# Performance work log

Hardware: AMD Instinct MI355X
Metric: run time of the kernel (lower is better)

The kernel has to match this reference:

```python
import jax, jax.numpy as jnp
import numpy as np

BS, LQ = 16, 300
D, NH = 256, 8
HD = D // NH
NLAYERS, DFF = 6, 1024
NLVL, NPTS = 4, 4
SUMP = NLVL * NPTS  # total sampling points per head
SPATIAL = [(80, 80), (40, 40), (20, 20), (10, 10)]
LEN_V = sum(h * w for h, w in SPATIAL)  # 8500
OFFSET_SCALE = 0.5


def layer_norm(x, g, b, eps=1e-5):
    m = jnp.mean(x, -1, keepdims=True)
    v = jnp.mean((x - m) ** 2, -1, keepdims=True)
    return (x - m) * jax.lax.rsqrt(v + eps) * g + b


def bilinear_gather(v, loc, Hs, Ws):
    # v: [bs, nh, Hs*Ws, hd]; loc: [bs, nh, N, 2] in [0,1] (x, y)
    # grid_sample bilinear, align_corners=False, zero padding
    x = loc[..., 0] * Ws - 0.5
    y = loc[..., 1] * Hs - 0.5
    x0 = jnp.floor(x); y0 = jnp.floor(y)
    x1 = x0 + 1.0; y1 = y0 + 1.0
    wx1 = x - x0; wx0 = 1.0 - wx1
    wy1 = y - y0; wy0 = 1.0 - wy1

    def corner(xi, yi, w):
        valid = (xi >= 0) & (xi <= Ws - 1) & (yi >= 0) & (yi <= Hs - 1)
        idx = (jnp.clip(yi, 0, Hs - 1) * Ws + jnp.clip(xi, 0, Ws - 1)).astype(jnp.int32)
        g = jnp.take_along_axis(v, idx[..., None], axis=2)  # [bs,nh,N,hd]
        return g * (w * valid)[..., None]

    return (corner(x0, y0, wx0 * wy0) + corner(x1, y0, wx1 * wy0)
            + corner(x0, y1, wx0 * wy1) + corner(x1, y1, wx1 * wy1))


def ms_deform_attn(value, loc, attn_w):
    # value [bs,LenV,D]; loc [bs,Lq,nh,SUMP,2]; attn_w [bs,Lq,nh,SUMP]
    bs, Lq = loc.shape[:2]
    v = value.reshape(bs, -1, NH, HD).transpose(0, 2, 1, 3)  # [bs,nh,LenV,hd]
    sizes = [h * w for h, w in SPATIAL]
    offs = np.cumsum([0] + sizes)
    outs = []
    for lvl, (Hs, Ws) in enumerate(SPATIAL):
        v_l = v[:, :, offs[lvl]:offs[lvl + 1], :]
        loc_l = loc[:, :, :, lvl * NPTS:(lvl + 1) * NPTS, :]
        loc_l = loc_l.transpose(0, 2, 1, 3, 4).reshape(bs, NH, Lq * NPTS, 2)
        s = bilinear_gather(v_l, loc_l, Hs, Ws).reshape(bs, NH, Lq, NPTS, HD)
        outs.append(s)
    samp = jnp.concatenate(outs, axis=3)  # [bs,nh,Lq,SUMP,hd]
    w = attn_w.transpose(0, 2, 1, 3)[..., None]
    out = jnp.sum(samp * w, axis=3)  # [bs,nh,Lq,hd]
    return out.transpose(0, 2, 1, 3).reshape(bs, Lq, D)


def mha(q_in, k_in, v_in, Wqkv, bqkv, Wo, bo):
    # torch nn.MultiheadAttention (batch_first), no dropout, no mask
    bs, Lq, _ = q_in.shape
    Wq, Wk, Wv = jnp.split(Wqkv, 3, axis=0)
    bq, bk, bv = jnp.split(bqkv, 3)
    q = (q_in @ Wq.T + bq).reshape(bs, Lq, NH, HD)
    k = (k_in @ Wk.T + bk).reshape(bs, -1, NH, HD)
    v = (v_in @ Wv.T + bv).reshape(bs, -1, NH, HD)
    scores = jnp.einsum('bqhd,bkhd->bhqk', q, k) / jnp.sqrt(jnp.float32(HD))
    a = jax.nn.softmax(scores, axis=-1)
    o = jnp.einsum('bhqk,bkhd->bqhd', a, v).reshape(bs, Lq, D)
    return o @ Wo.T + bo


def _forward(target, reference_points, value, query_pos_embed,
             attn_Wqkv, attn_bqkv, attn_Wo, attn_bo, n1_g, n1_b,
             so_W, so_b, aw_W, aw_b, g_W, g_b, gn_g, gn_b,
             l1_W, l1_b, l2_W, l2_b, n3_g, n3_b):
    bs, Lq = target.shape[:2]
    # num_points_scale = 1/n_points per point (all levels use NPTS points)
    nps = jnp.full((SUMP, 1), 1.0 / NPTS, dtype=target.dtype)
    t = target
    for i in range(NLAYERS):
        # self-attention
        q = t + query_pos_embed
        t2 = mha(q, q, t, attn_Wqkv[i], attn_bqkv[i], attn_Wo[i], attn_bo[i])
        t = layer_norm(t + t2, n1_g[i], n1_b[i])
        # MS deformable cross-attention (4-dim reference_points branch)
        qc = t + query_pos_embed
        so = (qc @ so_W[i].T + so_b[i]).reshape(bs, Lq, NH, SUMP, 2)
        aw = jax.nn.softmax((qc @ aw_W[i].T + aw_b[i]).reshape(bs, Lq, NH, SUMP), axis=-1)
        ref = reference_points[:, :, None, None, :]  # [bs,Lq,1,1,4]
        loc = ref[..., :2] + so * nps * ref[..., 2:] * OFFSET_SCALE
        t2 = ms_deform_attn(value, loc, aw)
        # gateway fusion
        gates = jax.nn.sigmoid(jnp.concatenate([t, t2], -1) @ g_W[i].T + g_b[i])
        g1, g2 = jnp.split(gates, 2, axis=-1)
        t = layer_norm(g1 * t + g2 * t2, gn_g[i], gn_b[i])
        # FFN
        t2 = jax.nn.relu(t @ l1_W[i].T + l1_b[i]) @ l2_W[i].T + l2_b[i]
        t = layer_norm(jnp.clip(t + t2, -65504.0, 65504.0), n3_g[i], n3_b[i])
    return t


def setup_inputs() -> dict:
    key = jax.random.key(0)
    ks = iter(jax.random.split(key, 40))

    def rn(shape, s=0.02):
        return jax.random.normal(next(ks), shape, dtype=jnp.float32) * s

    inp = {
        'target': jax.random.normal(next(ks), (BS, LQ, D), dtype=jnp.float32),
        'reference_points': jax.random.uniform(next(ks), (BS, LQ, 4), dtype=jnp.float32) * 0.5 + 0.25,
        'value': jax.random.normal(next(ks), (BS, LEN_V, D), dtype=jnp.float32),
        'query_pos_embed': jax.random.normal(next(ks), (BS, LQ, D), dtype=jnp.float32),
        'attn_Wqkv': rn((NLAYERS, 3 * D, D)),
        'attn_bqkv': jnp.zeros((NLAYERS, 3 * D), jnp.float32),
        'attn_Wo': rn((NLAYERS, D, D)),
        'attn_bo': jnp.zeros((NLAYERS, D), jnp.float32),
        'n1_g': jnp.ones((NLAYERS, D), jnp.float32),
        'n1_b': jnp.zeros((NLAYERS, D), jnp.float32),
        'so_W': rn((NLAYERS, NH * SUMP * 2, D)),
        'so_b': rn((NLAYERS, NH * SUMP * 2), 0.5),
        'aw_W': rn((NLAYERS, NH * SUMP, D)),
        'aw_b': jnp.zeros((NLAYERS, NH * SUMP), jnp.float32),
        'g_W': rn((NLAYERS, 2 * D, 2 * D)),
        'g_b': jnp.zeros((NLAYERS, 2 * D), jnp.float32),
        'gn_g': jnp.ones((NLAYERS, D), jnp.float32),
        'gn_b': jnp.zeros((NLAYERS, D), jnp.float32),
        'l1_W': rn((NLAYERS, DFF, D)),
        'l1_b': jnp.zeros((NLAYERS, DFF), jnp.float32),
        'l2_W': rn((NLAYERS, D, DFF)),
        'l2_b': jnp.zeros((NLAYERS, D), jnp.float32),
        'n3_g': jnp.ones((NLAYERS, D), jnp.float32),
        'n3_b': jnp.zeros((NLAYERS, D), jnp.float32),
    }
    return inp


def reference(target, reference_points, value, query_pos_embed,
              attn_Wqkv, attn_bqkv, attn_Wo, attn_bo, n1_g, n1_b,
              so_W, so_b, aw_W, aw_b, g_W, g_b, gn_g, gn_b,
              l1_W, l1_b, l2_W, l2_b, n3_g, n3_b):
    return _forward(target, reference_points, value, query_pos_embed,
                    attn_Wqkv, attn_bqkv, attn_Wo, attn_bo, n1_g, n1_b,
                    so_W, so_b, aw_W, aw_b, g_W, g_b, gn_g, gn_b,
                    l1_W, l1_b, l2_W, l2_b, n3_g, n3_b)
```

## Files before the change

kernel.cpp:

```cpp
#include <hip/hip_runtime.h>

#define BS 16
#define LQ 300
#define D 256
#define NH 8
#define HD 32
#define DFF 1024
#define ROWS (BS*LQ)
#define LEN_V 8500

typedef __attribute__((ext_vector_type(8))) short short8;
typedef __attribute__((ext_vector_type(4))) float f32x4;

__device__ __forceinline__ uint32_t bf16r(float x)
{
    const uint32_t u = __float_as_uint(x);
    return (u + 0x7fffu + ((u >> 16) & 1u)) >> 16;
}
__device__ __forceinline__ float lof(uint32_t p) { return __uint_as_float(p << 16); }
__device__ __forceinline__ float hif(uint32_t p) { return __uint_as_float(p & 0xffff0000u); }

template<int ACT>
__global__ __launch_bounds__(256)
void gemm_mfma(const float* __restrict__ A, int lda,
               const float* __restrict__ A2, int lda2, int ksplit,
               const float* __restrict__ W,
               const float* __restrict__ bias,
               float* __restrict__ C, int ldc, int coff,
               int K)
{
    __shared__ __align__(16) unsigned short As[64*64];
    __shared__ __align__(16) unsigned short Bs[64*64];
    const int tid  = threadIdx.x;
    const int bm   = blockIdx.x, bn = blockIdx.y;
    const int lane = tid & 63;
    const int w    = tid >> 6;
    const int wm   = (w >> 1) * 32, wn = (w & 1) * 32;
    const int fr   = lane & 15;
    const int fq   = lane >> 4;

    const int srow = tid >> 2;
    const int sg   = tid & 3;

    f32x4 acc[2][2] = {};

    for (int k0 = 0; k0 < K; k0 += 64) {
        float4 a0[2], a1[2], w0[2], w1[2];
#pragma unroll
        for (int p = 0; p < 2; ++p) {
            const int grp = sg + 4*p;
            const int kg  = k0 + grp*8;
            const float* Asrc = (A2 != nullptr && kg >= ksplit)
                ? (A2 + (size_t)(bm*64 + srow)*lda2 + (kg - ksplit))
                : (A  + (size_t)(bm*64 + srow)*lda  + kg);
            a0[p] = *reinterpret_cast<const float4*>(Asrc);
            a1[p] = *reinterpret_cast<const float4*>(Asrc + 4);
            const float* Wsrc = W + (size_t)(bn*64 + srow)*K + kg;
            w0[p] = *reinterpret_cast<const float4*>(Wsrc);
            w1[p] = *reinterpret_cast<const float4*>(Wsrc + 4);
        }
        __syncthreads();
#pragma unroll
        for (int p = 0; p < 2; ++p) {
            const int grp  = sg + 4*p;
            const int slot = grp ^ (srow & 7);
            uint32_t pk[4];
            pk[0] = bf16r(a0[p].x) | (bf16r(a0[p].y) << 16);
            pk[1] = bf16r(a0[p].z) | (bf16r(a0[p].w) << 16);
            pk[2] = bf16r(a1[p].x) | (bf16r(a1[p].y) << 16);
            pk[3] = bf16r(a1[p].z) | (bf16r(a1[p].w) << 16);
            *reinterpret_cast<uint4*>(&As[srow*64 + slot*8]) =
                make_uint4(pk[0], pk[1], pk[2], pk[3]);
            pk[0] = bf16r(w0[p].x) | (bf16r(w0[p].y) << 16);
            pk[1] = bf16r(w0[p].z) | (bf16r(w0[p].w) << 16);
            pk[2] = bf16r(w1[p].x) | (bf16r(w1[p].y) << 16);
            pk[3] = bf16r(w1[p].z) | (bf16r(w1[p].w) << 16);
            *reinterpret_cast<uint4*>(&Bs[srow*64 + slot*8]) =
                make_uint4(pk[0], pk[1], pk[2], pk[3]);
        }
        __syncthreads();
#pragma unroll
        for (int ks = 0; ks < 2; ++ks) {
            short8 af[2], bf[2];
#pragma unroll
            for (int fm = 0; fm < 2; ++fm) {
                const int row = wm + fm*16 + fr;
                const int slot = (ks*4 + fq) ^ (row & 7);
                af[fm] = *reinterpret_cast<const short8*>(&As[row*64 + slot*8]);
            }
#pragma unroll
            for (int fn = 0; fn < 2; ++fn) {
                const int row = wn + fn*16 + fr;
                const int slot = (ks*4 + fq) ^ (row & 7);
                bf[fn] = *reinterpret_cast<const short8*>(&Bs[row*64 + slot*8]);
            }
#pragma unroll
            for (int fm = 0; fm < 2; ++fm)
#pragma unroll
                for (int fn = 0; fn < 2; ++fn)
                    acc[fm][fn] = __builtin_amdgcn_mfma_f32_16x16x32_bf16(
                        af[fm], bf[fn], acc[fm][fn], 0, 0, 0);
        }
    }

#pragma unroll
    for (int fm = 0; fm < 2; ++fm)
#pragma unroll
        for (int fn = 0; fn < 2; ++fn) {
            const int col = bn*64 + wn + fn*16 + fr;
            const float bia = bias[col];
#pragma unroll
            for (int r = 0; r < 4; ++r) {
                const int row = bm*64 + wm + fm*16 + fq*4 + r;
                float v = acc[fm][fn][r] + bia;
                if (ACT == 1) v = fmaxf(v, 0.f);
                if (ACT == 2) v = 1.f / (1.f + __expf(-v));
                C[(size_t)row*ldc + coff + col] = v;
            }
        }
}

__global__ __launch_bounds__(256)
void add_pos(const float* __restrict__ t, const float* __restrict__ pos,
             float* __restrict__ q)
{
    const size_t idx = (size_t)blockIdx.x*256 + threadIdx.x;
    q[idx] = t[idx] + pos[idx];
}

__global__ __launch_bounds__(256)
void mha_block(const float* __restrict__ qkv, float* __restrict__ o)
{
    const int blk = blockIdx.x;
    const int quarter = blk & 3;
    const int bh = blk >> 2;
    const int b = bh >> 3, h = bh & 7;
    const int tid = threadIdx.x;
    const int lane = tid & 63;
    const int w = tid >> 6;

    __shared__ uint32_t Kp[16][320];
    __shared__ uint32_t Vp[150][32];
    __shared__ float    ws[4][304];
    const float* base = qkv + (size_t)b * LQ * 768;
    const int hc = h * 32;

    for (int idx = tid; idx < 300*16; idx += 256) {
        const int j = idx >> 4, d2 = idx & 15;
        const float2 kv = *reinterpret_cast<const float2*>(base + (size_t)j*768 + 256 + hc + 2*d2);
        Kp[d2][j] = (bf16r(kv.y) << 16) | bf16r(kv.x);
    }
    for (int idx = tid; idx < 16*20; idx += 256)
        Kp[idx/20][300 + idx%20] = 0;
    for (int idx = tid; idx < 150*32; idx += 256) {
        const int jp = idx >> 5, d = idx & 31;
        const float lo = base[(size_t)(2*jp  )*768 + 512 + hc + d];
        const float hi = base[(size_t)(2*jp+1)*768 + 512 + hc + d];
        Vp[jp][d] = (bf16r(hi) << 16) | bf16r(lo);
    }
    __syncthreads();

    const float scale = 0.17677669529663687f;
    const int qbase = quarter * 75;
    for (int il = w; il < 75; il += 4) {
        const int iq = qbase + il;
        const float2* qrow = reinterpret_cast<const float2*>(base + (size_t)iq*768 + hc);

        float s0=0.f, s1=0.f, s2=0.f, s3=0.f, s4=0.f;
#pragma unroll
        for (int d2 = 0; d2 < 16; ++d2) {
            const float2 q2 = qrow[d2];
            uint32_t k;
            k = Kp[d2][lane      ]; s0 += lof(k)*q2.x + hif(k)*q2.y;
            k = Kp[d2][lane +  64]; s1 += lof(k)*q2.x + hif(k)*q2.y;
            k = Kp[d2][lane + 128]; s2 += lof(k)*q2.x + hif(k)*q2.y;
            k = Kp[d2][lane + 192]; s3 += lof(k)*q2.x + hif(k)*q2.y;
            k = Kp[d2][lane + 256]; s4 += lof(k)*q2.x + hif(k)*q2.y;
        }
        s0 *= scale; s1 *= scale; s2 *= scale; s3 *= scale;
        s4 = (lane < 44) ? s4*scale : -3e38f;

        float m = fmaxf(fmaxf(fmaxf(s0,s1), fmaxf(s2,s3)), s4);
#pragma unroll
        for (int off = 32; off; off >>= 1) m = fmaxf(m, __shfl_xor(m, off));
        const float e0 = __expf(s0-m), e1 = __expf(s1-m), e2 = __expf(s2-m), e3 = __expf(s3-m);
        const float e4 = (lane < 44) ? __expf(s4-m) : 0.f;
        float sum = e0+e1+e2+e3+e4;
#pragma unroll
        for (int off = 32; off; off >>= 1) sum += __shfl_xor(sum, off);
        const float inv = 1.f / sum;
        ws[w][lane      ] = e0;
        ws[w][lane +  64] = e1;
        ws[w][lane + 128] = e2;
        ws[w][lane + 192] = e3;
        if (lane < 44) ws[w][lane + 256] = e4;

        const int half = lane >> 5, d = lane & 31;
        float acc = 0.f;
#pragma unroll 5
        for (int jp = half*75; jp < half*75 + 75; ++jp) {
            const float2 w2 = *reinterpret_cast<const float2*>(&ws[w][2*jp]);
            const uint32_t v2 = Vp[jp][d];
            acc += lof(v2)*w2.x + hif(v2)*w2.y;
        }
        acc += __shfl_down(acc, 32);
        if (lane < 32)
            o[((size_t)(b*LQ + iq))*256 + hc + d] = acc * inv;
    }
}

__device__ __forceinline__ float blk_sum(float v, float* red)
{
#pragma unroll
    for (int off = 32; off; off >>= 1) v += __shfl_down(v, off, 64);
    const int lane = threadIdx.x & 63, w = threadIdx.x >> 6;
    if (lane == 0) red[w] = v;
    __syncthreads();
    const float s = red[0] + red[1] + red[2] + red[3];
    __syncthreads();
    return s;
}

__global__ __launch_bounds__(256)
void ln_res_pos(const float* __restrict__ t, const float* __restrict__ t2,
                const float* __restrict__ g, const float* __restrict__ bb,
                const float* __restrict__ pos,
                float* __restrict__ t_out, float* __restrict__ q_out)
{
    __shared__ float red[4];
    const size_t idx = (size_t)blockIdx.x*256 + threadIdx.x;
    const float x = t[idx] + t2[idx];
    const float mean = blk_sum(x, red) * (1.f/256.f);
    const float c = x - mean;
    const float var = blk_sum(c*c, red) * (1.f/256.f);
    const float y = c * rsqrtf(var + 1e-5f) * g[threadIdx.x] + bb[threadIdx.x];
    t_out[idx] = y;
    q_out[idx] = y + pos[idx];
}

__global__ __launch_bounds__(256)
void gate_ln(const float* __restrict__ t, const float* __restrict__ t2,
             const float* __restrict__ gates,
             const float* __restrict__ g, const float* __restrict__ bb,
             float* __restrict__ t_out)
{
    __shared__ float red[4];
    const int row = blockIdx.x, dd = threadIdx.x;
    const size_t idx = (size_t)row*256 + dd;
    const float g1 = gates[(size_t)row*512 + dd];
    const float g2 = gates[(size_t)row*512 + 256 + dd];
    const float x = g1 * t[idx] + g2 * t2[idx];
    const float mean = blk_sum(x, red) * (1.f/256.f);
    const float c = x - mean;
    const float var = blk_sum(c*c, red) * (1.f/256.f);
    t_out[idx] = c * rsqrtf(var + 1e-5f) * g[dd] + bb[dd];
}

__global__ __launch_bounds__(256)
void ln_clip(const float* __restrict__ t, const float* __restrict__ t2,
             const float* __restrict__ g, const float* __restrict__ bb,
             float* __restrict__ outp)
{
    __shared__ float red[4];
    const size_t idx = (size_t)blockIdx.x*256 + threadIdx.x;
    float x = t[idx] + t2[idx];
    x = fminf(fmaxf(x, -65504.f), 65504.f);
    const float mean = blk_sum(x, red) * (1.f/256.f);
    const float c = x - mean;
    const float var = blk_sum(c*c, red) * (1.f/256.f);
    outp[idx] = c * rsqrtf(var + 1e-5f) * g[threadIdx.x] + bb[threadIdx.x];
}

__global__ __launch_bounds__(128)
void aw_softmax(float* __restrict__ aw)
{
    const int bq = blockIdx.x;
    const int tid = threadIdx.x;
    const float v = aw[(size_t)bq*128 + tid];
    float m = v;
#pragma unroll
    for (int off = 8; off; off >>= 1) m = fmaxf(m, __shfl_xor(m, off, 16));
    const float e = __expf(v - m);
    float s = e;
#pragma unroll
    for (int off = 8; off; off >>= 1) s += __shfl_xor(s, off, 16);
    aw[(size_t)bq*128 + tid] = e / s;
}

__global__ __launch_bounds__(256)
void deform_attn(const float* __restrict__ value, const float* __restrict__ refp,
                 const float* __restrict__ so, const float* __restrict__ aw,
                 float* __restrict__ outp)
{
    const int bq = blockIdx.x;
    const int b  = bq / LQ;
    const int tid = threadIdx.x;
    __shared__ int   s_idx[128][4];
    __shared__ float s_w[128][4];
    if (tid < 128) {
        const int hp = tid;
        const int p  = hp & 15;
        const int lvl = p >> 2;
        const float Wl = (lvl == 0) ? 80.f : (lvl == 1) ? 40.f : (lvl == 2) ? 20.f : 10.f;
        const float Hl = Wl;
        const int off  = (lvl == 0) ? 0 : (lvl == 1) ? 6400 : (lvl == 2) ? 8000 : 8400;
        const float cx = refp[bq*4+0], cy = refp[bq*4+1];
        const float rw = refp[bq*4+2], rh = refp[bq*4+3];
        const float lx = cx + so[(size_t)bq*256 + hp*2 + 0] * rw * 0.125f;
        const float ly = cy + so[(size_t)bq*256 + hp*2 + 1] * rh * 0.125f;
        const float x = lx * Wl - 0.5f;
        const float y = ly * Hl - 0.5f;
        const float x0 = floorf(x), y0 = floorf(y);
        const float wx1 = x - x0, wx0 = 1.f - wx1;
        const float wy1 = y - y0, wy0 = 1.f - wy1;
        const float a = aw[(size_t)bq*128 + hp];
        const float xs[2]  = {x0, x0 + 1.f}, ys[2]  = {y0, y0 + 1.f};
        const float wxs[2] = {wx0, wx1},     wys[2] = {wy0, wy1};
#pragma unroll
        for (int cyi = 0; cyi < 2; ++cyi)
#pragma unroll
            for (int cxi = 0; cxi < 2; ++cxi) {
                const float xi = xs[cxi], yi = ys[cyi];
                const bool valid = (xi >= 0.f) && (xi <= Wl - 1.f) &&
                                   (yi >= 0.f) && (yi <= Hl - 1.f);
                const float xc = fminf(fmaxf(xi, 0.f), Wl - 1.f);
                const float yc = fminf(fmaxf(yi, 0.f), Hl - 1.f);
                const int c = cyi*2 + cxi;
                s_idx[hp][c] = (int)(yc*Wl + xc) + off;
                s_w[hp][c]   = valid ? (wxs[cxi]*wys[cyi]*a) : 0.f;
            }
    }
    __syncthreads();
    const int h = tid >> 5, d = tid & 31;
    const int col = h*32 + d;
    const float* vb = value + (size_t)b * LEN_V * 256;
    float acc = 0.f;
#pragma unroll
    for (int p = 0; p < 16; ++p) {
        const int hp = (h << 4) | p;
#pragma unroll
        for (int c = 0; c < 4; ++c)
            acc += s_w[hp][c] * vb[(size_t)s_idx[hp][c]*256 + col];
    }
    outp[(size_t)bq*256 + col] = acc;
}

extern "C" void kernel_launch(void* const* d_in, const int* in_sizes, int n_in,
                              void* d_out, int out_size, void* d_ws, size_t ws_size,
                              hipStream_t stream)
{
    (void)in_sizes; (void)n_in; (void)out_size; (void)ws_size;
    const float* target = (const float*)d_in[0];
    const float* refp   = (const float*)d_in[1];
    const float* value  = (const float*)d_in[2];
    const float* qpos   = (const float*)d_in[3];
    const float* Wqkv   = (const float*)d_in[4];
    const float* bqkv   = (const float*)d_in[5];
    const float* Wo     = (const float*)d_in[6];
    const float* bo     = (const float*)d_in[7];
    const float* n1g    = (const float*)d_in[8];
    const float* n1b    = (const float*)d_in[9];
    const float* soW    = (const float*)d_in[10];
    const float* sob    = (const float*)d_in[11];
    const float* awW    = (const float*)d_in[12];
    const float* awb    = (const float*)d_in[13];
    const float* gW     = (const float*)d_in[14];
    const float* gb     = (const float*)d_in[15];
    const float* gng    = (const float*)d_in[16];
    const float* gnb    = (const float*)d_in[17];
    const float* l1W    = (const float*)d_in[18];
    const float* l1b    = (const float*)d_in[19];
    const float* l2W    = (const float*)d_in[20];
    const float* l2b    = (const float*)d_in[21];
    const float* n3g    = (const float*)d_in[22];
    const float* n3b    = (const float*)d_in[23];

    float* p = (float*)d_ws;
    float* t_buf = p;  p += (size_t)ROWS*D;
    float* q_buf = p;  p += (size_t)ROWS*D;
    float* qkv   = p;
    float* o_buf = qkv + (size_t)ROWS*768;
    float* hid   = qkv;
    p += (size_t)ROWS*(768 + 256);
    float* t2    = p;  p += (size_t)ROWS*D;
    float* so_b  = p;  p += (size_t)ROWS*D;
    float* aw_b  = p;  p += (size_t)ROWS*128;
    float* gates = p;  p += (size_t)ROWS*512;

    hipMemcpyAsync(t_buf, target, (size_t)ROWS*D*sizeof(float),
                   hipMemcpyDeviceToDevice, stream);

    for (int i = 0; i < 6; ++i) {
        const float* Wqkv_i = Wqkv + (size_t)i*768*256;
        const float* bqkv_i = bqkv + (size_t)i*768;
        const float* Wo_i   = Wo   + (size_t)i*256*256;
        const float* bo_i   = bo   + (size_t)i*256;
        const float* n1g_i  = n1g  + (size_t)i*256;
        const float* n1b_i  = n1b  + (size_t)i*256;
        const float* soW_i  = soW  + (size_t)i*256*256;
        const float* sob_i  = sob  + (size_t)i*256;
        const float* awW_i  = awW  + (size_t)i*128*256;
        const float* awb_i  = awb  + (size_t)i*128;
        const float* gW_i   = gW   + (size_t)i*512*512;
        const float* gb_i   = gb   + (size_t)i*512;
        const float* gng_i  = gng  + (size_t)i*256;
        const float* gnb_i  = gnb  + (size_t)i*256;
        const float* l1W_i  = l1W  + (size_t)i*1024*256;
        const float* l1b_i  = l1b  + (size_t)i*1024;
        const float* l2W_i  = l2W  + (size_t)i*256*1024;
        const float* l2b_i  = l2b  + (size_t)i*256;
        const float* n3g_i  = n3g  + (size_t)i*256;
        const float* n3b_i  = n3b  + (size_t)i*256;

        add_pos<<<ROWS, 256, 0, stream>>>(t_buf, qpos, q_buf);
        gemm_mfma<0><<<dim3(75, 8), 256, 0, stream>>>(q_buf, 256, nullptr, 0, 0,
            Wqkv_i, bqkv_i, qkv, 768, 0, 256);
        gemm_mfma<0><<<dim3(75, 4), 256, 0, stream>>>(t_buf, 256, nullptr, 0, 0,
            Wqkv_i + 512*256, bqkv_i + 512, qkv, 768, 512, 256);
        mha_block<<<BS*NH*4, 256, 0, stream>>>(qkv, o_buf);
        gemm_mfma<0><<<dim3(75, 4), 256, 0, stream>>>(o_buf, 256, nullptr, 0, 0,
            Wo_i, bo_i, t2, 256, 0, 256);
        ln_res_pos<<<ROWS, 256, 0, stream>>>(t_buf, t2, n1g_i, n1b_i, qpos, t_buf, q_buf);

        gemm_mfma<0><<<dim3(75, 4), 256, 0, stream>>>(q_buf, 256, nullptr, 0, 0,
            soW_i, sob_i, so_b, 256, 0, 256);
        gemm_mfma<0><<<dim3(75, 2), 256, 0, stream>>>(q_buf, 256, nullptr, 0, 0,
            awW_i, awb_i, aw_b, 128, 0, 256);
        aw_softmax<<<ROWS, 128, 0, stream>>>(aw_b);
        deform_attn<<<ROWS, 256, 0, stream>>>(value, refp, so_b, aw_b, t2);

        gemm_mfma<2><<<dim3(75, 8), 256, 0, stream>>>(t_buf, 256, t2, 256, 256,
            gW_i, gb_i, gates, 512, 0, 512);
        gate_ln<<<ROWS, 256, 0, stream>>>(t_buf, t2, gates, gng_i, gnb_i, t_buf);

        gemm_mfma<1><<<dim3(75, 16), 256, 0, stream>>>(t_buf, 256, nullptr, 0, 0,
            l1W_i, l1b_i, hid, 1024, 0, 256);
        gemm_mfma<0><<<dim3(75, 4), 256, 0, stream>>>(hid, 1024, nullptr, 0, 0,
            l2W_i, l2b_i, t2, 256, 0, 1024);
        ln_clip<<<ROWS, 256, 0, stream>>>(t_buf, t2, n3g_i, n3b_i,
                                          (i == 5) ? (float*)d_out : t_buf);
    }
}
```

Before: 1.396 ms.

## Keep activations, weights and value in bf16 and fuse softmax into deform attention

Weights and the value tensor are converted to bf16 once per call. Activations feeding the GEMMs are written as bf16 by the producing kernels (LN, MHA, deform_attn, qkv and FFN hidden), so GEMMs load bf16 directly with no per-tile conversion. The sampling-offset and attention-weight GEMMs are merged into one launch, the attention-weight softmax moves into deform_attn, and the add_pos kernel is folded into the LN epilogues. This cuts global memory traffic and launch count, at the cost of conversion kernels run on every call, a larger workspace, and added bf16 rounding of intermediates.

Result: slower. 1.810 ms (+29.6%).

```diff
diff --git a/kernel.cpp b/kernel.cpp
--- a/kernel.cpp
+++ b/kernel.cpp
@@ -11,6 +11,7 @@
 
 typedef __attribute__((ext_vector_type(8))) short short8;
 typedef __attribute__((ext_vector_type(4))) float f32x4;
+typedef unsigned short ushort_t;
 
 __device__ __forceinline__ uint32_t bf16r(float x)
 {
@@ -20,17 +21,16 @@
 __device__ __forceinline__ float lof(uint32_t p) { return __uint_as_float(p << 16); }
 __device__ __forceinline__ float hif(uint32_t p) { return __uint_as_float(p & 0xffff0000u); }
 
-template<int ACT>
-__global__ __launch_bounds__(256)
-void gemm_mfma(const float* __restrict__ A, int lda,
-               const float* __restrict__ A2, int lda2, int ksplit,
-               const float* __restrict__ W,
-               const float* __restrict__ bias,
-               float* __restrict__ C, int ldc, int coff,
-               int K)
-{
-    __shared__ __align__(16) unsigned short As[64*64];
-    __shared__ __align__(16) unsigned short Bs[64*64];
+template<int ACT, int OUTBF>
+__global__ __launch_bounds__(256)
+void gemm_bf(const ushort_t* __restrict__ A, int lda,
+             const ushort_t* __restrict__ A2, int lda2, int ksplit,
+             const ushort_t* __restrict__ W,
+             const float* __restrict__ bias, const float* __restrict__ bias2, int bsplit,
+             void* __restrict__ Cv, int ldc, int coff, int K)
+{
+    __shared__ __align__(16) ushort_t As[64*64];
+    __shared__ __align__(16) ushort_t Bs[64*64];
     const int tid  = threadIdx.x;
     const int bm   = blockIdx.x, bn = blockIdx.y;
     const int lane = tid & 63;
@@ -45,38 +45,23 @@
     f32x4 acc[2][2] = {};
 
     for (int k0 = 0; k0 < K; k0 += 64) {
-        float4 a0[2], a1[2], w0[2], w1[2];
+        uint4 aval[2], wval[2];
 #pragma unroll
         for (int p = 0; p < 2; ++p) {
-            const int grp = sg + 4*p;
-            const int kg  = k0 + grp*8;
-            const float* Asrc = (A2 != nullptr && kg >= ksplit)
+            const int slot = sg + 4*p;
+            const int kg   = k0 + slot*8;
+            const ushort_t* Asrc = (A2 != nullptr && kg >= ksplit)
                 ? (A2 + (size_t)(bm*64 + srow)*lda2 + (kg - ksplit))
                 : (A  + (size_t)(bm*64 + srow)*lda  + kg);
-            a0[p] = *reinterpret_cast<const float4*>(Asrc);
-            a1[p] = *reinterpret_cast<const float4*>(Asrc + 4);
-            const float* Wsrc = W + (size_t)(bn*64 + srow)*K + kg;
-            w0[p] = *reinterpret_cast<const float4*>(Wsrc);
-            w1[p] = *reinterpret_cast<const float4*>(Wsrc + 4);
+            aval[p] = *reinterpret_cast<const uint4*>(Asrc);
+            wval[p] = *reinterpret_cast<const uint4*>(W + (size_t)(bn*64 + srow)*K + kg);
         }
         __syncthreads();
 #pragma unroll
         for (int p = 0; p < 2; ++p) {
-            const int grp  = sg + 4*p;
-            const int slot = grp ^ (srow & 7);
-            uint32_t pk[4];
-            pk[0] = bf16r(a0[p].x) | (bf16r(a0[p].y) << 16);
-            pk[1] = bf16r(a0[p].z) | (bf16r(a0[p].w) << 16);
-            pk[2] = bf16r(a1[p].x) | (bf16r(a1[p].y) << 16);
-            pk[3] = bf16r(a1[p].z) | (bf16r(a1[p].w) << 16);
-            *reinterpret_cast<uint4*>(&As[srow*64 + slot*8]) =
-                make_uint4(pk[0], pk[1], pk[2], pk[3]);
-            pk[0] = bf16r(w0[p].x) | (bf16r(w0[p].y) << 16);
-            pk[1] = bf16r(w0[p].z) | (bf16r(w0[p].w) << 16);
-            pk[2] = bf16r(w1[p].x) | (bf16r(w1[p].y) << 16);
-            pk[3] = bf16r(w1[p].z) | (bf16r(w1[p].w) << 16);
-            *reinterpret_cast<uint4*>(&Bs[srow*64 + slot*8]) =
-                make_uint4(pk[0], pk[1], pk[2], pk[3]);
+            const int slot = (sg + 4*p) ^ (srow & 7);
+            *reinterpret_cast<uint4*>(&As[srow*64 + slot*8]) = aval[p];
+            *reinterpret_cast<uint4*>(&Bs[srow*64 + slot*8]) = wval[p];
         }
         __syncthreads();
 #pragma unroll
@@ -108,28 +93,55 @@
 #pragma unroll
         for (int fn = 0; fn < 2; ++fn) {
             const int col = bn*64 + wn + fn*16 + fr;
-            const float bia = bias[col];
+            const float bia = (bias2 != nullptr && col >= bsplit)
+                            ? bias2[col - bsplit] : bias[col];
 #pragma unroll
             for (int r = 0; r < 4; ++r) {
                 const int row = bm*64 + wm + fm*16 + fq*4 + r;
                 float v = acc[fm][fn][r] + bia;
                 if (ACT == 1) v = fmaxf(v, 0.f);
                 if (ACT == 2) v = 1.f / (1.f + __expf(-v));
-                C[(size_t)row*ldc + coff + col] = v;
+                if (OUTBF) ((ushort_t*)Cv)[(size_t)row*ldc + coff + col] = (ushort_t)bf16r(v);
+                else       ((float*)Cv)  [(size_t)row*ldc + coff + col] = v;
             }
         }
 }
 
 __global__ __launch_bounds__(256)
-void add_pos(const float* __restrict__ t, const float* __restrict__ pos,
-             float* __restrict__ q)
+void prep0(const float* __restrict__ target, const float* __restrict__ pos,
+           float* __restrict__ t, ushort_t* __restrict__ tbf, ushort_t* __restrict__ qbf)
 {
     const size_t idx = (size_t)blockIdx.x*256 + threadIdx.x;
-    q[idx] = t[idx] + pos[idx];
-}
-
-__global__ __launch_bounds__(256)
-void mha_block(const float* __restrict__ qkv, float* __restrict__ o)
+    const float v = target[idx];
+    t[idx]   = v;
+    tbf[idx] = (ushort_t)bf16r(v);
+    qbf[idx] = (ushort_t)bf16r(v + pos[idx]);
+}
+
+__global__ __launch_bounds__(256)
+void cvt_strided(const float* __restrict__ src, ushort_t* __restrict__ dst,
+                 int per_layer, int dst_stride, int dst_off, int nlayers)
+{
+    const int total = per_layer * nlayers;
+    for (int i = blockIdx.x*256 + threadIdx.x; i < total; i += gridDim.x*256) {
+        const int l = i / per_layer, r = i - l*per_layer;
+        dst[(size_t)l*dst_stride + dst_off + r] = (ushort_t)bf16r(src[i]);
+    }
+}
+
+__global__ __launch_bounds__(256)
+void cvt_flat4(const float* __restrict__ src, ushort_t* __restrict__ dst, int n4)
+{
+    for (int i = blockIdx.x*256 + threadIdx.x; i < n4; i += gridDim.x*256) {
+        const float4 v = reinterpret_cast<const float4*>(src)[i];
+        ushort_t o[4] = {(ushort_t)bf16r(v.x), (ushort_t)bf16r(v.y),
+                         (ushort_t)bf16r(v.z), (ushort_t)bf16r(v.w)};
+        *reinterpret_cast<uint2*>(dst + (size_t)i*4) = *reinterpret_cast<uint2*>(o);
+    }
+}
+
+__global__ __launch_bounds__(256)
+void mha_block(const ushort_t* __restrict__ qkv, ushort_t* __restrict__ o)
 {
     const int blk = blockIdx.x;
     const int quarter = blk & 3;
@@ -142,21 +154,20 @@
     __shared__ uint32_t Kp[16][320];
     __shared__ uint32_t Vp[150][32];
     __shared__ float    ws[4][304];
-    const float* base = qkv + (size_t)b * LQ * 768;
+    const ushort_t* base = qkv + (size_t)b * LQ * 768;
     const int hc = h * 32;
 
     for (int idx = tid; idx < 300*16; idx += 256) {
         const int j = idx >> 4, d2 = idx & 15;
-        const float2 kv = *reinterpret_cast<const float2*>(base + (size_t)j*768 + 256 + hc + 2*d2);
-        Kp[d2][j] = (bf16r(kv.y) << 16) | bf16r(kv.x);
+        Kp[d2][j] = *reinterpret_cast<const uint32_t*>(base + (size_t)j*768 + 256 + hc + 2*d2);
     }
     for (int idx = tid; idx < 16*20; idx += 256)
         Kp[idx/20][300 + idx%20] = 0;
     for (int idx = tid; idx < 150*32; idx += 256) {
         const int jp = idx >> 5, d = idx & 31;
-        const float lo = base[(size_t)(2*jp  )*768 + 512 + hc + d];
-        const float hi = base[(size_t)(2*jp+1)*768 + 512 + hc + d];
-        Vp[jp][d] = (bf16r(hi) << 16) | bf16r(lo);
+        const uint32_t lo = base[(size_t)(2*jp  )*768 + 512 + hc + d];
+        const uint32_t hi = base[(size_t)(2*jp+1)*768 + 512 + hc + d];
+        Vp[jp][d] = (hi << 16) | lo;
     }
     __syncthreads();
 
@@ -164,18 +175,19 @@
     const int qbase = quarter * 75;
     for (int il = w; il < 75; il += 4) {
         const int iq = qbase + il;
-        const float2* qrow = reinterpret_cast<const float2*>(base + (size_t)iq*768 + hc);
+        const uint32_t* qrow = reinterpret_cast<const uint32_t*>(base + (size_t)iq*768 + hc);
 
         float s0=0.f, s1=0.f, s2=0.f, s3=0.f, s4=0.f;
 #pragma unroll
         for (int d2 = 0; d2 < 16; ++d2) {
-            const float2 q2 = qrow[d2];
+            const uint32_t qp = qrow[d2];
+            const float qx = lof(qp), qy = hif(qp);
             uint32_t k;
-            k = Kp[d2][lane      ]; s0 += lof(k)*q2.x + hif(k)*q2.y;
-            k = Kp[d2][lane +  64]; s1 += lof(k)*q2.x + hif(k)*q2.y;
-            k = Kp[d2][lane + 128]; s2 += lof(k)*q2.x + hif(k)*q2.y;
-            k = Kp[d2][lane + 192]; s3 += lof(k)*q2.x + hif(k)*q2.y;
-            k = Kp[d2][lane + 256]; s4 += lof(k)*q2.x + hif(k)*q2.y;
+            k = Kp[d2][lane      ]; s0 += lof(k)*qx + hif(k)*qy;
+            k = Kp[d2][lane +  64]; s1 += lof(k)*qx + hif(k)*qy;
+            k = Kp[d2][lane + 128]; s2 += lof(k)*qx + hif(k)*qy;
+            k = Kp[d2][lane + 192]; s3 += lof(k)*qx + hif(k)*qy;
+            k = Kp[d2][lane + 256]; s4 += lof(k)*qx + hif(k)*qy;
         }
         s0 *= scale; s1 *= scale; s2 *= scale; s3 *= scale;
         s4 = (lane < 44) ? s4*scale : -3e38f;
@@ -205,7 +217,7 @@
         }
         acc += __shfl_down(acc, 32);
         if (lane < 32)
-            o[((size_t)(b*LQ + iq))*256 + hc + d] = acc * inv;
+            o[((size_t)(b*LQ + iq))*256 + hc + d] = (ushort_t)bf16r(acc * inv);
     }
 }
 
@@ -225,7 +237,8 @@
 void ln_res_pos(const float* __restrict__ t, const float* __restrict__ t2,
                 const float* __restrict__ g, const float* __restrict__ bb,
                 const float* __restrict__ pos,
-                float* __restrict__ t_out, float* __restrict__ q_out)
+                float* __restrict__ t_out, ushort_t* __restrict__ tbf,
+                ushort_t* __restrict__ qbf)
 {
     __shared__ float red[4];
     const size_t idx = (size_t)blockIdx.x*256 + threadIdx.x;
@@ -235,14 +248,15 @@
     const float var = blk_sum(c*c, red) * (1.f/256.f);
     const float y = c * rsqrtf(var + 1e-5f) * g[threadIdx.x] + bb[threadIdx.x];
     t_out[idx] = y;
-    q_out[idx] = y + pos[idx];
+    tbf[idx]   = (ushort_t)bf16r(y);
+    qbf[idx]   = (ushort_t)bf16r(y + pos[idx]);
 }
 
 __global__ __launch_bounds__(256)
 void gate_ln(const float* __restrict__ t, const float* __restrict__ t2,
              const float* __restrict__ gates,
              const float* __restrict__ g, const float* __restrict__ bb,
-             float* __restrict__ t_out)
+             float* __restrict__ t_out, ushort_t* __restrict__ tbf)
 {
     __shared__ float red[4];
     const int row = blockIdx.x, dd = threadIdx.x;
@@ -253,13 +267,17 @@
     const float mean = blk_sum(x, red) * (1.f/256.f);
     const float c = x - mean;
     const float var = blk_sum(c*c, red) * (1.f/256.f);
-    t_out[idx] = c * rsqrtf(var + 1e-5f) * g[dd] + bb[dd];
+    const float y = c * rsqrtf(var + 1e-5f) * g[dd] + bb[dd];
+    t_out[idx] = y;
+    tbf[idx]   = (ushort_t)bf16r(y);
 }
 
 __global__ __launch_bounds__(256)
 void ln_clip(const float* __restrict__ t, const float* __restrict__ t2,
              const float* __restrict__ g, const float* __restrict__ bb,
-             float* __restrict__ outp)
+             const float* __restrict__ pos,
+             float* __restrict__ outp, ushort_t* __restrict__ tbf,
+             ushort_t* __restrict__ qbf)
 {
     __shared__ float red[4];
     const size_t idx = (size_t)blockIdx.x*256 + threadIdx.x;
@@ -268,29 +286,19 @@
     const float mean = blk_sum(x, red) * (1.f/256.f);
     const float c = x - mean;
     const float var = blk_sum(c*c, red) * (1.f/256.f);
-    outp[idx] = c * rsqrtf(var + 1e-5f) * g[threadIdx.x] + bb[threadIdx.x];
-}
-
-__global__ __launch_bounds__(128)
-void aw_softmax(float* __restrict__ aw)
-{
-    const int bq = blockIdx.x;
-    const int tid = threadIdx.x;
-    const float v = aw[(size_t)bq*128 + tid];
-    float m = v;
-#pragma unroll
-    for (int off = 8; off; off >>= 1) m = fmaxf(m, __shfl_xor(m, off, 16));
-    const float e = __expf(v - m);
-    float s = e;
-#pragma unroll
-    for (int off = 8; off; off >>= 1) s += __shfl_xor(s, off, 16);
-    aw[(size_t)bq*128 + tid] = e / s;
-}
-
-__global__ __launch_bounds__(256)
-void deform_attn(const float* __restrict__ value, const float* __restrict__ refp,
-                 const float* __restrict__ so, const float* __restrict__ aw,
-                 float* __restrict__ outp)
+    const float y = c * rsqrtf(var + 1e-5f) * g[threadIdx.x] + bb[threadIdx.x];
+    outp[idx] = y;
+    if (tbf != nullptr) {
+        tbf[idx] = (ushort_t)bf16r(y);
+        qbf[idx] = (ushort_t)bf16r(y + pos[idx]);
+    }
+}
+
+template<int VBF>
+__global__ __launch_bounds__(256)
+void deform_attn(const void* __restrict__ value_p, const float* __restrict__ refp,
+                 const float* __restrict__ soaw,
+                 float* __restrict__ out_f, ushort_t* __restrict__ out_bf)
 {
     const int bq = blockIdx.x;
     const int b  = bq / LQ;
@@ -304,16 +312,25 @@
         const float Wl = (lvl == 0) ? 80.f : (lvl == 1) ? 40.f : (lvl == 2) ? 20.f : 10.f;
         const float Hl = Wl;
         const int off  = (lvl == 0) ? 0 : (lvl == 1) ? 6400 : (lvl == 2) ? 8000 : 8400;
+        const float logit = soaw[(size_t)bq*384 + 256 + hp];
+        float m = logit;
+#pragma unroll
+        for (int o = 8; o; o >>= 1) m = fmaxf(m, __shfl_xor(m, o, 16));
+        const float e = __expf(logit - m);
+        float ssum = e;
+#pragma unroll
+        for (int o = 8; o; o >>= 1) ssum += __shfl_xor(ssum, o, 16);
+        const float a = e / ssum;
+
         const float cx = refp[bq*4+0], cy = refp[bq*4+1];
         const float rw = refp[bq*4+2], rh = refp[bq*4+3];
-        const float lx = cx + so[(size_t)bq*256 + hp*2 + 0] * rw * 0.125f;
-        const float ly = cy + so[(size_t)bq*256 + hp*2 + 1] * rh * 0.125f;
+        const float lx = cx + soaw[(size_t)bq*384 + hp*2    ] * rw * 0.125f;
+        const float ly = cy + soaw[(size_t)bq*384 + hp*2 + 1] * rh * 0.125f;
         const float x = lx * Wl - 0.5f;
         const float y = ly * Hl - 0.5f;
         const float x0 = floorf(x), y0 = floorf(y);
         const float wx1 = x - x0, wx0 = 1.f - wx1;
         const float wy1 = y - y0, wy0 = 1.f - wy1;
-        const float a = aw[(size_t)bq*128 + hp];
         const float xs[2]  = {x0, x0 + 1.f}, ys[2]  = {y0, y0 + 1.f};
         const float wxs[2] = {wx0, wx1},     wys[2] = {wy0, wy1};
 #pragma unroll
@@ -333,23 +350,36 @@
     __syncthreads();
     const int h = tid >> 5, d = tid & 31;
     const int col = h*32 + d;
-    const float* vb = value + (size_t)b * LEN_V * 256;
     float acc = 0.f;
-#pragma unroll
-    for (int p = 0; p < 16; ++p) {
-        const int hp = (h << 4) | p;
-#pragma unroll
-        for (int c = 0; c < 4; ++c)
-            acc += s_w[hp][c] * vb[(size_t)s_idx[hp][c]*256 + col];
-    }
-    outp[(size_t)bq*256 + col] = acc;
+    if (VBF) {
+        const ushort_t* vb = (const ushort_t*)value_p + (size_t)b * LEN_V * 256;
+#pragma unroll
+        for (int p = 0; p < 16; ++p) {
+            const int hp = (h << 4) | p;
+#pragma unroll
+            for (int c = 0; c < 4; ++c)
+                acc += s_w[hp][c] *
+                       __uint_as_float(((uint32_t)vb[(size_t)s_idx[hp][c]*256 + col]) << 16);
+        }
+    } else {
+        const float* vb = (const float*)value_p + (size_t)b * LEN_V * 256;
+#pragma unroll
+        for (int p = 0; p < 16; ++p) {
+            const int hp = (h << 4) | p;
+#pragma unroll
+            for (int c = 0; c < 4; ++c)
+                acc += s_w[hp][c] * vb[(size_t)s_idx[hp][c]*256 + col];
+        }
+    }
+    out_f[(size_t)bq*256 + col]  = acc;
+    out_bf[(size_t)bq*256 + col] = (ushort_t)bf16r(acc);
 }
 
 extern "C" void kernel_launch(void* const* d_in, const int* in_sizes, int n_in,
                               void* d_out, int out_size, void* d_ws, size_t ws_size,
                               hipStream_t stream)
 {
-    (void)in_sizes; (void)n_in; (void)out_size; (void)ws_size;
+    (void)in_sizes; (void)n_in; (void)out_size;
     const float* target = (const float*)d_in[0];
     const float* refp   = (const float*)d_in[1];
     const float* value  = (const float*)d_in[2];
@@ -375,69 +405,98 @@
     const float* n3g    = (const float*)d_in[22];
     const float* n3b    = (const float*)d_in[23];
 
-    float* p = (float*)d_ws;
-    float* t_buf = p;  p += (size_t)ROWS*D;
-    float* q_buf = p;  p += (size_t)ROWS*D;
-    float* qkv   = p;
-    float* o_buf = qkv + (size_t)ROWS*768;
-    float* hid   = qkv;
-    p += (size_t)ROWS*(768 + 256);
-    float* t2    = p;  p += (size_t)ROWS*D;
-    float* so_b  = p;  p += (size_t)ROWS*D;
-    float* aw_b  = p;  p += (size_t)ROWS*128;
-    float* gates = p;  p += (size_t)ROWS*512;
-
-    hipMemcpyAsync(t_buf, target, (size_t)ROWS*D*sizeof(float),
-                   hipMemcpyDeviceToDevice, stream);
+    char* base = (char*)d_ws;
+    size_t used = 0;
+    auto carve = [&](size_t bytes) -> void* {
+        void* r = base + used;
+        used += (bytes + 255) & ~(size_t)255;
+        return r;
+    };
+    float*    t_buf  = (float*)   carve((size_t)ROWS*256*4);
+    float*    t2     = (float*)   carve((size_t)ROWS*256*4);
+    float*    gates  = (float*)   carve((size_t)ROWS*512*4);
+    ushort_t* hid_bf = (ushort_t*)gates;
+    float*    soaw   = (float*)   carve((size_t)ROWS*384*4);
+    ushort_t* qkv_bf = (ushort_t*)soaw;
+    ushort_t* q_bf   = (ushort_t*)carve((size_t)ROWS*256*2);
+    ushort_t* t_bf   = (ushort_t*)carve((size_t)ROWS*256*2);
+    ushort_t* t2d_bf = (ushort_t*)carve((size_t)ROWS*256*2);
+    ushort_t* o_bf   = (ushort_t*)carve((size_t)ROWS*256*2);
+    ushort_t* w_bf   = (ushort_t*)carve((size_t)6881280*2);
+
+    ushort_t* wqkv_bf = w_bf;
+    ushort_t* wo_bf   = wqkv_bf + 6*196608;
+    ushort_t* wsoaw_bf= wo_bf   + 6*65536;
+    ushort_t* wg_bf   = wsoaw_bf+ 6*98304;
+    ushort_t* wl1_bf  = wg_bf   + 6*262144;
+    ushort_t* wl2_bf  = wl1_bf  + 6*262144;
+
+    const size_t val_elems = (size_t)BS*LEN_V*256;
+    ushort_t* val_bf = nullptr;
+    if (ws_size - used >= val_elems*2 + 256)
+        val_bf = (ushort_t*)carve(val_elems*2);
+
+    cvt_strided<<<2048, 256, 0, stream>>>(Wqkv, wqkv_bf, 196608, 196608, 0, 6);
+    cvt_strided<<<1024, 256, 0, stream>>>(Wo,   wo_bf,   65536,  65536,  0, 6);
+    cvt_strided<<<1024, 256, 0, stream>>>(soW,  wsoaw_bf,65536,  98304,  0, 6);
+    cvt_strided<<<512,  256, 0, stream>>>(awW,  wsoaw_bf,32768,  98304,  65536, 6);
+    cvt_strided<<<2048, 256, 0, stream>>>(gW,   wg_bf,   262144, 262144, 0, 6);
+    cvt_strided<<<2048, 256, 0, stream>>>(l1W,  wl1_bf,  262144, 262144, 0, 6);
+    cvt_strided<<<2048, 256, 0, stream>>>(l2W,  wl2_bf,  262144, 262144, 0, 6);
+    if (val_bf)
+        cvt_flat4<<<2048, 256, 0, stream>>>(value, val_bf, (int)(val_elems/4));
+    prep0<<<ROWS, 256, 0, stream>>>(target, qpos, t_buf, t_bf, q_bf);
 
     for (int i = 0; i < 6; ++i) {
-        const float* Wqkv_i = Wqkv + (size_t)i*768*256;
         const float* bqkv_i = bqkv + (size_t)i*768;
-        const float* Wo_i   = Wo   + (size_t)i*256*256;
         const float* bo_i   = bo   + (size_t)i*256;
         const float* n1g_i  = n1g  + (size_t)i*256;
         const float* n1b_i  = n1b  + (size_t)i*256;
-        const float* soW_i  = soW  + (size_t)i*256*256;
         const float* sob_i  = sob  + (size_t)i*256;
-        const float* awW_i  = awW  + (size_t)i*128*256;
         const float* awb_i  = awb  + (size_t)i*128;
-        const float* gW_i   = gW   + (size_t)i*512*512;
         const float* gb_i   = gb   + (size_t)i*512;
         const float* gng_i  = gng  + (size_t)i*256;
         const float* gnb_i  = gnb  + (size_t)i*256;
-        const float* l1W_i  = l1W  + (size_t)i*1024*256;
         const float* l1b_i  = l1b  + (size_t)i*1024;
-        const float* l2W_i  = l2W  + (size_t)i*256*1024;
         const float* l2b_i  = l2b  + (size_t)i*256;
         const float* n3g_i  = n3g  + (size_t)i*256;
         const float* n3b_i  = n3b  + (size_t)i*256;
 
-        add_pos<<<ROWS, 256, 0, stream>>>(t_buf, qpos, q_buf);
-        gemm_mfma<0><<<dim3(75, 8), 256, 0, stream>>>(q_buf, 256, nullptr, 0, 0,
-            Wqkv_i, bqkv_i, qkv, 768, 0, 256);
-        gemm_mfma<0><<<dim3(75, 4), 256, 0, stream>>>(t_buf, 256, nullptr, 0, 0,
-            Wqkv_i + 512*256, bqkv_i + 512, qkv, 768, 512, 256);
-        mha_block<<<BS*NH*4, 256, 0, stream>>>(qkv, o_buf);
-        gemm_mfma<0><<<dim3(75, 4), 256, 0, stream>>>(o_buf, 256, nullptr, 0, 0,
-            Wo_i, bo_i, t2, 256, 0, 256);
-        ln_res_pos<<<ROWS, 256, 0, stream>>>(t_buf, t2, n1g_i, n1b_i, qpos, t_buf, q_buf);
-
-        gemm_mfma<0><<<dim3(75, 4), 256, 0, stream>>>(q_buf, 256, nullptr, 0, 0,
-            soW_i, sob_i, so_b, 256, 0, 256);
-        gemm_mfma<0><<<dim3(75, 2), 256, 0, stream>>>(q_buf, 256, nullptr, 0, 0,
-            awW_i, awb_i, aw_b, 128, 0, 256);
-        aw_softmax<<<ROWS, 128, 0, stream>>>(aw_b);
-        deform_attn<<<ROWS, 256, 0, stream>>>(value, refp, so_b, aw_b, t2);
-
-        gemm_mfma<2><<<dim3(75, 8), 256, 0, stream>>>(t_buf, 256, t2, 256, 256,
-            gW_i, gb_i, gates, 512, 0, 512);
-        gate_ln<<<ROWS, 256, 0, stream>>>(t_buf, t2, gates, gng_i, gnb_i, t_buf);
-
-        gemm_mfma<1><<<dim3(75, 16), 256, 0, stream>>>(t_buf, 256, nullptr, 0, 0,
-            l1W_i, l1b_i, hid, 1024, 0, 256);
-        gemm_mfma<0><<<dim3(75, 4), 256, 0, stream>>>(hid, 1024, nullptr, 0, 0,
-            l2W_i, l2b_i, t2, 256, 0, 1024);
-        ln_clip<<<ROWS, 256, 0, stream>>>(t_buf, t2, n3g_i, n3b_i,
-                                          (i == 5) ? (float*)d_out : t_buf);
-    }
-}
+        const ushort_t* wqkv_i = wqkv_bf  + (size_t)i*196608;
+        const ushort_t* wo_i   = wo_bf    + (size_t)i*65536;
+        const ushort_t* wsa_i  = wsoaw_bf + (size_t)i*98304;
+        const ushort_t* wg_i   = wg_bf    + (size_t)i*262144;
+        const ushort_t* wl1_i  = wl1_bf   + (size_t)i*262144;
+        const ushort_t* wl2_i  = wl2_bf   + (size_t)i*262144;
+
+        gemm_bf<0,1><<<dim3(75, 8), 256, 0, stream>>>(q_bf, 256, nullptr, 0, 0,
+            wqkv_i, bqkv_i, nullptr, 0, qkv_bf, 768, 0, 256);
+        gemm_bf<0,1><<<dim3(75, 4), 256, 0, stream>>>(t_bf, 256, nullptr, 0, 0,
+            wqkv_i + 512*256, bqkv_i + 512, nullptr, 0, qkv_bf, 768, 512, 256);
+        mha_block<<<BS*NH*4, 256, 0, stream>>>(qkv_bf, o_bf);
+        gemm_bf<0,0><<<dim3(75, 4), 256, 0, stream>>>(o_bf, 256, nullptr, 0, 0,
+            wo_i, bo_i, nullptr, 0, t2, 256, 0, 256);
+        ln_res_pos<<<ROWS, 256, 0, stream>>>(t_buf, t2, n1g_i, n1b_i, qpos,
+                                             t_buf, t_bf, q_bf);
+
+        gemm_bf<0,0><<<dim3(75, 6), 256, 0, stream>>>(q_bf, 256, nullptr, 0, 0,
+            wsa_i, sob_i, awb_i, 256, soaw, 384, 0, 256);
+        if (val_bf)
+            deform_attn<1><<<ROWS, 256, 0, stream>>>(val_bf, refp, soaw, t2, t2d_bf);
+        else
+            deform_attn<0><<<ROWS, 256, 0, stream>>>(value, refp, soaw, t2, t2d_bf);
+
+        gemm_bf<2,0><<<dim3(75, 8), 256, 0, stream>>>(t_bf, 256, t2d_bf, 256, 256,
+            wg_i, gb_i, nullptr, 0, gates, 512, 0, 512);
+        gate_ln<<<ROWS, 256, 0, stream>>>(t_buf, t2, gates, gng_i, gnb_i, t_buf, t_bf);
+
+        gemm_bf<1,1><<<dim3(75, 16), 256, 0, stream>>>(t_bf, 256, nullptr, 0, 0,
+            wl1_i, l1b_i, nullptr, 0, hid_bf, 1024, 0, 256);
+        gemm_bf<0,0><<<dim3(75, 4), 256, 0, stream>>>(hid_bf, 1024, nullptr, 0, 0,
+            wl2_i, l2b_i, nullptr, 0, t2, 256, 0, 1024);
+        ln_clip<<<ROWS, 256, 0, stream>>>(t_buf, t2, n3g_i, n3b_i, qpos,
+                                          (i == 5) ? (float*)d_out : t_buf,
+                                          (i < 5) ? t_bf : nullptr,
+                                          (i < 5) ? q_bf : nullptr);
+    }
+}
```
